# Optimization experiments

Hardware: AMD Instinct MI355X
Metric: run time of the kernel (lower is better)

## Reference

```python
import jax, jax.numpy as jnp
import numpy as np

N, C, H, W = 16, 512, 32, 32
NH = 8            # num_heads
HD = C // NH      # head dim c = 64
G = C // 4        # GroupNorm groups = 128
EPS = 1e-5


def conv1x1(X, Wt, b):
    # 1x1 Conv2d == per-pixel linear over channels
    return jnp.einsum('oc,nchw->nohw', Wt, X) + b[None, :, None, None]


def setup_inputs() -> dict:
    key = jax.random.key(0)
    ks = jax.random.split(key, 9)
    s = 0.02
    inp = {
        'X': jax.random.normal(ks[0], (N, C, H, W), jnp.float32),
        'Wq': jax.random.normal(ks[1], (C, C), jnp.float32) * s,
        'bq': jax.random.normal(ks[2], (C,), jnp.float32) * s,
        'Wk': jax.random.normal(ks[3], (C, C), jnp.float32) * s,
        'bk': jax.random.normal(ks[4], (C,), jnp.float32) * s,
        'Wv': jax.random.normal(ks[5], (C, C), jnp.float32) * s,
        'bv': jax.random.normal(ks[6], (C,), jnp.float32) * s,
        'Wo': jax.random.normal(ks[7], (C, C), jnp.float32) * s,
        'bo': jax.random.normal(ks[8], (C,), jnp.float32) * s,
        'gn_w': jnp.ones((C,), jnp.float32),
        'gn_b': jnp.zeros((C,), jnp.float32),
    }
    return inp


def reference(X, Wq, bq, Wk, bk, Wv, bv, Wo, bo, gn_w, gn_b):
    # NOTE: original torch code does  K, Q, V = (Q_conv(X), K_conv(X), V_conv(X))
    # i.e. K gets the Q_conv weights and Q gets the K_conv weights; mirror that.
    K = conv1x1(X, Wq, bq)
    Q = conv1x1(X, Wk, bk)
    V = conv1x1(X, Wv, bv)

    d = H * W
    Kh = K.reshape(N, NH, HD, d)  # [n,h,c,d]
    Qh = Q.reshape(N, NH, HD, d)
    Vh = V.reshape(N, NH, HD, d)

    # softmax-free channel attention: (Q^T K) then V (Q^T K)^T
    A = jnp.einsum('nhcd,nhcD->nhdD', Qh, Kh)   # [n,h,d,d]
    O = jnp.einsum('nhdD,nhcD->nhcd', A, Vh)    # [n,h,c,d]

    O = O.reshape(N, C, H, W)
    O = conv1x1(O, Wo, bo)

    # GroupNorm(G, C) with affine, eps=1e-5
    Og = O.reshape(N, G, C // G, H, W)
    mu = Og.mean(axis=(2, 3, 4), keepdims=True)
    var = Og.var(axis=(2, 3, 4), keepdims=True)
    On = ((Og - mu) * jax.lax.rsqrt(var + EPS)).reshape(N, C, H, W)
    On = On * gn_w[None, :, None, None] + gn_b[None, :, None, None]

    return On + X
```

## Files before the change

### kernel.cpp

```cpp
#include <hip/hip_runtime.h>
#include <hip/hip_bf16.h>

typedef __attribute__((ext_vector_type(8))) short s8v;
typedef __attribute__((ext_vector_type(4))) short s4v;
typedef __attribute__((ext_vector_type(4))) float f32x4;

#define MFMA_BF16 __builtin_amdgcn_mfma_f32_16x16x32_bf16

__device__ inline void gload_lds16(const __hip_bfloat16* g, __hip_bfloat16* l) {
  __builtin_amdgcn_global_load_lds(
      (const __attribute__((address_space(1))) void*)g,
      (__attribute__((address_space(3))) void*)l, 16, 0, 0);
}

__device__ inline short f2bs(float x) {
  __hip_bfloat16 b = __float2bfloat16(x);
  return *reinterpret_cast<short*>(&b);
}

__device__ inline void storeC(float* p, float v) { *p = v; }
__device__ inline void storeC(__hip_bfloat16* p, float v) { *p = __float2bfloat16(v); }

__global__ __launch_bounds__(256) void prep(const float* __restrict__ X,
                                            __hip_bfloat16* __restrict__ XT,
                                            const float* __restrict__ Wq,
                                            const float* __restrict__ Wv,
                                            const float* __restrict__ Wk,
                                            const float* __restrict__ Wo,
                                            const float* __restrict__ bq,
                                            const float* __restrict__ bv,
                                            __hip_bfloat16* __restrict__ WA,
                                            __hip_bfloat16* __restrict__ WkT,
                                            __hip_bfloat16* __restrict__ WOb,
                                            float* __restrict__ biasKV) {
  const int tid = threadIdx.x;
  if (blockIdx.z == 16) {
    const int blk = blockIdx.y * 16 + blockIdx.x;
#pragma unroll
    for (int t = 0; t < 8; ++t) {
      const int i = (blk * 8 + t) * 256 + tid;
      WA[i] = __float2bfloat16(Wq[i]);
      WA[262144 + i] = __float2bfloat16(Wv[i]);
      WOb[i] = __float2bfloat16(Wo[i]);
      WkT[i] = __float2bfloat16(Wk[(i & 511) * 512 + (i >> 9)]);
      if (i < 512) { biasKV[i] = bq[i]; biasKV[512 + i] = bv[i]; }
    }
    return;
  }
  __shared__ float tl[64][65];
  const int n = blockIdx.z;
  const int c0 = blockIdx.y * 64, p0 = blockIdx.x * 64;
  const int lr = tid >> 4, lc4 = (tid & 15) * 4;
  const float* Xp = X + ((long)n * 512 + c0) * 1024 + p0;
#pragma unroll
  for (int i = 0; i < 4; ++i) {
    const int ch = i * 16 + lr;
    const float4 v = *(const float4*)&Xp[(long)ch * 1024 + lc4];
    tl[ch][lc4 + 0] = v.x; tl[ch][lc4 + 1] = v.y;
    tl[ch][lc4 + 2] = v.z; tl[ch][lc4 + 3] = v.w;
  }
  __syncthreads();
  __hip_bfloat16* XTp = XT + ((long)n * 1024 + p0) * 512 + c0;
#pragma unroll
  for (int i = 0; i < 4; ++i) {
    const int px = i * 16 + lr;
    s4v o;
#pragma unroll
    for (int e = 0; e < 4; ++e) o[e] = f2bs(tl[lc4 + e][px]);
    *(s4v*)&XTp[(long)px * 512 + lc4] = o;
  }
}

template <typename OutT, bool BROW>
__global__ __launch_bounds__(256) void gemm_nt(
    const __hip_bfloat16* __restrict__ A, long strideA,
    const __hip_bfloat16* __restrict__ B, long strideB,
    OutT* __restrict__ C, long strideC, int K, int ldc,
    const float* __restrict__ brow, long strideBrow) {
  A += blockIdx.z * strideA;
  B += blockIdx.z * strideB;
  C += blockIdx.z * strideC;
  const int m0 = blockIdx.y * 128;
  const int n0 = blockIdx.x * 128;
  const int tid = threadIdx.x;
  const int wid = tid >> 6, lane = tid & 63;
  const int wm = wid >> 1, wn = wid & 1;

  __shared__ __hip_bfloat16 As[128 * 64];
  __shared__ __hip_bfloat16 Bs[128 * 64];

  f32x4 acc[4][4] = {};

  const __hip_bfloat16* gA0 = A + (long)(m0 + wid * 32 + (lane >> 3)) * K + (lane & 7) * 8;
  const __hip_bfloat16* gB0 = B + (long)(n0 + wid * 32 + (lane >> 3)) * K + (lane & 7) * 8;

  for (int k0 = 0; k0 < K; k0 += 64) {
#pragma unroll
    for (int t = 0; t < 4; ++t) {
      gload_lds16(gA0 + (long)t * 8 * K + k0, &As[(wid * 32 + t * 8) * 64]);
      gload_lds16(gB0 + (long)t * 8 * K + k0, &Bs[(wid * 32 + t * 8) * 64]);
    }
    __syncthreads();
#pragma unroll
    for (int ks = 0; ks < 2; ++ks) {
      const int koff = ks * 32 + (lane >> 4) * 8;
      s8v a[4], b[4];
#pragma unroll
      for (int i = 0; i < 4; ++i)
        a[i] = *(const s8v*)&As[(wm * 64 + i * 16 + (lane & 15)) * 64 + koff];
#pragma unroll
      for (int j = 0; j < 4; ++j)
        b[j] = *(const s8v*)&Bs[(wn * 64 + j * 16 + (lane & 15)) * 64 + koff];
#pragma unroll
      for (int i = 0; i < 4; ++i)
#pragma unroll
        for (int j = 0; j < 4; ++j)
          acc[i][j] = MFMA_BF16(a[i], b[j], acc[i][j], 0, 0, 0);
    }
    __syncthreads();
  }

  const int cr = (lane >> 4) * 4;
  const int cc = lane & 15;
#pragma unroll
  for (int i = 0; i < 4; ++i) {
#pragma unroll
    for (int r = 0; r < 4; ++r) {
      const int gm = m0 + wm * 64 + i * 16 + cr + r;
      const float rb = BROW ? brow[blockIdx.z * strideBrow + gm] : 0.f;
#pragma unroll
      for (int j = 0; j < 4; ++j) {
        const int gn = n0 + wn * 64 + j * 16 + cc;
        storeC(&C[(long)gm * ldc + gn], acc[i][j][r] + rb);
      }
    }
  }
}

__global__ __launch_bounds__(512) void gemm_vkT(const __hip_bfloat16* __restrict__ V,
                                                const __hip_bfloat16* __restrict__ Kk,
                                                __hip_bfloat16* __restrict__ Mt) {
  const int n = blockIdx.x >> 3, h = blockIdx.x & 7;
  const int tid = threadIdx.x, wid = tid >> 6, lane = tid & 63;
  f32x4 acc[4][4] = {};
  const long colbase = (long)n * 1024 + wid * 128 + (lane >> 4) * 8;
  const __hip_bfloat16* Vb = V + (long)(h * 64 + (lane & 15)) * 16384 + colbase;
  const __hip_bfloat16* Kb = Kk + (long)(h * 64 + (lane & 15)) * 16384 + colbase;
#pragma unroll
  for (int kk = 0; kk < 128; kk += 32) {
    s8v a[4], b[4];
#pragma unroll
    for (int i = 0; i < 4; ++i) a[i] = *(const s8v*)(Vb + (long)i * 16 * 16384 + kk);
#pragma unroll
    for (int j = 0; j < 4; ++j) b[j] = *(const s8v*)(Kb + (long)j * 16 * 16384 + kk);
#pragma unroll
    for (int i = 0; i < 4; ++i)
#pragma unroll
      for (int j = 0; j < 4; ++j) acc[i][j] = MFMA_BF16(a[i], b[j], acc[i][j], 0, 0, 0);
  }
  __shared__ float part[4][4096];
  const int cr = (lane >> 4) * 4, cc = lane & 15;
  if (wid < 4) {
#pragma unroll
    for (int i = 0; i < 4; ++i)
#pragma unroll
      for (int r = 0; r < 4; ++r)
#pragma unroll
        for (int j = 0; j < 4; ++j)
          part[wid][(i * 16 + cr + r) * 64 + j * 16 + cc] = acc[i][j][r];
  }
  __syncthreads();
  if (wid >= 4) {
#pragma unroll
    for (int i = 0; i < 4; ++i)
#pragma unroll
      for (int r = 0; r < 4; ++r)
#pragma unroll
        for (int j = 0; j < 4; ++j)
          part[wid - 4][(i * 16 + cr + r) * 64 + j * 16 + cc] += acc[i][j][r];
  }
  __syncthreads();
  __hip_bfloat16* outp = Mt + ((long)n * 8 + h) * 4096;
  for (int e = tid; e < 4096; e += 512) {
    const float sum = part[0][e] + part[1][e] + part[2][e] + part[3][e];
    outp[(e & 63) * 64 + (e >> 6)] = __float2bfloat16(sum);
  }
}

__global__ __launch_bounds__(256) void wchain(const __hip_bfloat16* __restrict__ WOb,
                                              const __hip_bfloat16* __restrict__ WkT,
                                              const __hip_bfloat16* __restrict__ Mt,
                                              const float* __restrict__ bk,
                                              const float* __restrict__ bo,
                                              __hip_bfloat16* __restrict__ WPP,
                                              float* __restrict__ b2out) {
  const int c0 = blockIdx.x * 128, o0 = blockIdx.y * 128, n = blockIdx.z;
  const int tid = threadIdx.x, wid = tid >> 6, lane = tid & 63;
  const int wm = wid >> 1, wn = wid & 1;
  const int cr = (lane >> 4) * 4, cc = lane & 15;

  __shared__ __hip_bfloat16 WoS[128 * 64];
  __shared__ __hip_bfloat16 WkS[128 * 64];
  __shared__ __hip_bfloat16 MtS[64 * 64];
  __shared__ __hip_bfloat16 W1S[128 * 64];
  __shared__ float bkS[512];

  if (tid < 128) *(float4*)&bkS[tid * 4] = *(const float4*)&bk[tid * 4];

  f32x4 acc2[4][4] = {};
  float bacc = 0.f;
  const int r8 = lane >> 3, b8 = (lane & 7) * 8;

  for (int h = 0; h < 8; ++h) {
#pragma unroll
    for (int t = 0; t < 4; ++t) {
      const int row = wid * 32 + t * 8;
      gload_lds16(WOb + (long)(o0 + row + r8) * 512 + h * 64 + b8, &WoS[row * 64]);
      gload_lds16(WkT + (long)(c0 + row + r8) * 512 + h * 64 + b8, &WkS[row * 64]);
    }
    {
      const __hip_bfloat16* mg = Mt + ((long)n * 8 + h) * 4096;
      gload_lds16(mg + wid * 512 + lane * 8, &MtS[wid * 512]);
      gload_lds16(mg + 2048 + wid * 512 + lane * 8, &MtS[2048 + wid * 512]);
    }
    __syncthreads();

    f32x4 acc1[2][4] = {};
#pragma unroll
    for (int ks = 0; ks < 2; ++ks) {
      const int ko = ks * 32 + (lane >> 4) * 8;
      s8v aj[2], bw[4];
#pragma unroll
      for (int i = 0; i < 2; ++i)
        aj[i] = *(const s8v*)&MtS[(wn * 32 + i * 16 + cc) * 64 + ko];
#pragma unroll
      for (int t = 0; t < 4; ++t)
        bw[t] = *(const s8v*)&WoS[(wm * 64 + t * 16 + cc) * 64 + ko];
#pragma unroll
      for (int i = 0; i < 2; ++i)
#pragma unroll
        for (int t = 0; t < 4; ++t)
          acc1[i][t] = MFMA_BF16(aj[i], bw[t], acc1[i][t], 0, 0, 0);
    }
#pragma unroll
    for (int i = 0; i < 2; ++i)
#pragma unroll
      for (int t = 0; t < 4; ++t) {
        const int o = wm * 64 + t * 16 + cc;
        const int jb = wn * 32 + i * 16 + cr;
        s4v p;
#pragma unroll
        for (int r = 0; r < 4; ++r) p[r] = f2bs(acc1[i][t][r]);
        *(s4v*)((char*)W1S + ((o * 128 + jb * 2) ^ ((o & 7) << 4))) = p;
      }
    __syncthreads();

#pragma unroll
    for (int ks = 0; ks < 2; ++ks) {
      const int ko = ks * 32 + (lane >> 4) * 8;
      s8v a2[4], bw[4];
#pragma unroll
      for (int i = 0; i < 4; ++i) {
        const int o = wm * 64 + i * 16 + cc;
        a2[i] = *(const s8v*)((char*)W1S + ((o * 128 + ko * 2) ^ ((o & 7) << 4)));
      }
#pragma unroll
      for (int t = 0; t < 4; ++t)
        bw[t] = *(const s8v*)&WkS[(wn * 64 + t * 16 + cc) * 64 + ko];
#pragma unroll
      for (int i = 0; i < 4; ++i)
#pragma unroll
        for (int t = 0; t < 4; ++t)
          acc2[i][t] = MFMA_BF16(a2[i], bw[t], acc2[i][t], 0, 0, 0);
    }

    if (c0 == 0) {
      const int o = tid >> 1, half = tid & 1;
      float s = 0.f;
#pragma unroll
      for (int q = 0; q < 4; ++q) {
        const int jb = half * 64 + q * 16;
        const s8v w = *(const s8v*)((char*)W1S + ((o * 128 + jb) ^ ((o & 7) << 4)));
        const __hip_bfloat16* wb = (const __hip_bfloat16*)&w;
#pragma unroll
        for (int e = 0; e < 8; ++e)
          s += __bfloat162float(wb[e]) * bkS[h * 64 + half * 32 + q * 8 + e];
      }
      bacc += s;
    }
    __syncthreads();
  }

#pragma unroll
  for (int i = 0; i < 4; ++i)
#pragma unroll
    for (int r = 0; r < 4; ++r)
#pragma unroll
      for (int t = 0; t < 4; ++t)
        WPP[((long)n * 512 + o0 + wm * 64 + i * 16 + cr + r) * 512 +
            c0 + wn * 64 + t * 16 + cc] = __float2bfloat16(acc2[i][t][r]);
  if (c0 == 0) {
    const float tot = bacc + __shfl_xor(bacc, 1);
    if ((tid & 1) == 0) {
      const int o = tid >> 1;
      b2out[n * 512 + o0 + o] = tot + bo[o0 + o];
    }
  }
}

__global__ __launch_bounds__(256) void gn_res(const __hip_bfloat16* __restrict__ Y,
                                              const float* __restrict__ X,
                                              const float* __restrict__ gw,
                                              const float* __restrict__ gb,
                                              float* __restrict__ out) {
  const int n = blockIdx.x >> 7, g = blockIdx.x & 127;
  const long base = ((long)n * 512 + g * 4) * 1024;
  const int tid = threadIdx.x;
  float v[16];
  float s = 0.f, s2 = 0.f;
#pragma unroll
  for (int i = 0; i < 2; ++i) {
    const s8v x = *(const s8v*)&Y[base + ((long)(i * 256 + tid)) * 8];
#pragma unroll
    for (int e = 0; e < 8; ++e) {
      const float f = __bfloat162float(((const __hip_bfloat16*)&x)[e]);
      v[i * 8 + e] = f;
      s += f;
      s2 += f * f;
    }
  }
#pragma unroll
  for (int off = 32; off; off >>= 1) {
    s += __shfl_down(s, off);
    s2 += __shfl_down(s2, off);
  }
  __shared__ float rs[8];
  const int wid = tid >> 6, lane = tid & 63;
  if (lane == 0) { rs[wid] = s; rs[4 + wid] = s2; }
  __syncthreads();
  if (tid == 0) {
    const float ts = rs[0] + rs[1] + rs[2] + rs[3];
    const float t2 = rs[4] + rs[5] + rs[6] + rs[7];
    const float mu = ts * (1.f / 4096.f);
    const float var = t2 * (1.f / 4096.f) - mu * mu;
    rs[0] = mu;
    rs[1] = rsqrtf(var + 1e-5f);
  }
  __syncthreads();
  const float mu = rs[0], rstd = rs[1];
#pragma unroll
  for (int i = 0; i < 2; ++i) {
    const int chunk = i * 256 + tid;
    const long e0 = base + (long)chunk * 8;
    const int c = g * 4 + (chunk >> 7);
    const float sc = rstd * gw[c], sh = gb[c];
    const float4 x0 = *(const float4*)&X[e0];
    const float4 x1 = *(const float4*)&X[e0 + 4];
    float4 o0, o1;
    o0.x = (v[i * 8 + 0] - mu) * sc + sh + x0.x;
    o0.y = (v[i * 8 + 1] - mu) * sc + sh + x0.y;
    o0.z = (v[i * 8 + 2] - mu) * sc + sh + x0.z;
    o0.w = (v[i * 8 + 3] - mu) * sc + sh + x0.w;
    o1.x = (v[i * 8 + 4] - mu) * sc + sh + x1.x;
    o1.y = (v[i * 8 + 5] - mu) * sc + sh + x1.y;
    o1.z = (v[i * 8 + 6] - mu) * sc + sh + x1.z;
    o1.w = (v[i * 8 + 7] - mu) * sc + sh + x1.w;
    *(float4*)&out[e0] = o0;
    *(float4*)&out[e0 + 4] = o1;
  }
}

extern "C" void kernel_launch(void* const* d_in, const int* in_sizes, int n_in,
                              void* d_out, int out_size, void* d_ws, size_t ws_size,
                              hipStream_t stream) {
  const float* X  = (const float*)d_in[0];
  const float* Wq = (const float*)d_in[1];
  const float* bq = (const float*)d_in[2];
  const float* Wk = (const float*)d_in[3];
  const float* bk = (const float*)d_in[4];
  const float* Wv = (const float*)d_in[5];
  const float* bv = (const float*)d_in[6];
  const float* Wo = (const float*)d_in[7];
  const float* bo = (const float*)d_in[8];
  const float* gw = (const float*)d_in[9];
  const float* gb = (const float*)d_in[10];
  float* out = (float*)d_out;

  char* ws = (char*)d_ws;
  __hip_bfloat16* XT  = (__hip_bfloat16*)(ws + 0);
  __hip_bfloat16* KV  = (__hip_bfloat16*)(ws + 16777216);
  __hip_bfloat16* Y   = (__hip_bfloat16*)(ws + 16777216);
  __hip_bfloat16* WPP = (__hip_bfloat16*)(ws + 58720256);
  __hip_bfloat16* Mt  = (__hip_bfloat16*)(ws + 67108864);
  __hip_bfloat16* WA  = (__hip_bfloat16*)(ws + 68157440);
  __hip_bfloat16* WkT = (__hip_bfloat16*)(ws + 69206016);
  __hip_bfloat16* WOb = (__hip_bfloat16*)(ws + 69730304);
  float*          bKV = (float*)(ws + 70254592);
  float*          b2  = (float*)(ws + 70258688);

  prep<<<dim3(16, 8, 17), 256, 0, stream>>>(X, XT, Wq, Wv, Wk, Wo, bq, bv,
                                            WA, WkT, WOb, bKV);
  gemm_nt<__hip_bfloat16, true><<<dim3(128, 8, 1), 256, 0, stream>>>(
      WA, 0, XT, 0, KV, 0, 512, 16384, bKV, 0);
  gemm_vkT<<<128, 512, 0, stream>>>(KV + (long)512 * 16384, KV, Mt);
  wchain<<<dim3(4, 4, 16), 256, 0, stream>>>(WOb, WkT, Mt, bk, bo, WPP, b2);
  gemm_nt<__hip_bfloat16, true><<<dim3(8, 4, 16), 256, 0, stream>>>(
      WPP, 262144, XT, 524288, Y, 524288, 512, 1024, b2, 512);
  gn_res<<<2048, 256, 0, stream>>>(Y, X, gw, gb, out);
}
```

Measured before the change: 117.2 us.

## Split VK^T reduction across two blocks, XCD-swizzle QKV GEMM, narrow final GEMM tiles

gemm_vkT now launches twice as many blocks. Each one reduces half of the spatial dimension and writes fp32 partials, and wchain sums the two halves and converts them to bf16 when loading into LDS. The first GEMM gets a 1D grid with an XCD-aware block remap so that blocks sharing data land on the same chiplet's L2. The final batched GEMM uses 128x64 tiles, giving twice as many blocks and better CU occupancy. The costs are extra fp32 partial traffic and a smaller MFMA work-per-load ratio in the narrowed GEMM.

```diff
diff --git a/kernel.cpp b/kernel.cpp
--- a/kernel.cpp
+++ b/kernel.cpp
@@ -71,50 +71,61 @@
   }
 }
 
-template <typename OutT, bool BROW>
+template <typename OutT, bool BROW, int NJ, int SWZ>
 __global__ __launch_bounds__(256) void gemm_nt(
     const __hip_bfloat16* __restrict__ A, long strideA,
     const __hip_bfloat16* __restrict__ B, long strideB,
     OutT* __restrict__ C, long strideC, int K, int ldc,
     const float* __restrict__ brow, long strideBrow) {
-  A += blockIdx.z * strideA;
-  B += blockIdx.z * strideB;
-  C += blockIdx.z * strideC;
-  const int m0 = blockIdx.y * 128;
-  const int n0 = blockIdx.x * 128;
+  int bx, by, bz;
+  if (SWZ == 1) {
+    const int id = blockIdx.x;
+    const int xcd = id & 7, local = id >> 3;
+    bx = xcd * 16 + (local >> 3);
+    by = local & 7;
+    bz = 0;
+  } else {
+    bx = blockIdx.x; by = blockIdx.y; bz = blockIdx.z;
+  }
+  A += bz * strideA;
+  B += bz * strideB;
+  C += bz * strideC;
+  const int m0 = by * 128;
+  const int n0 = bx * (32 * NJ);
   const int tid = threadIdx.x;
   const int wid = tid >> 6, lane = tid & 63;
   const int wm = wid >> 1, wn = wid & 1;
 
   __shared__ __hip_bfloat16 As[128 * 64];
-  __shared__ __hip_bfloat16 Bs[128 * 64];
-
-  f32x4 acc[4][4] = {};
+  __shared__ __hip_bfloat16 Bs[32 * NJ * 64];
+
+  f32x4 acc[4][NJ] = {};
 
   const __hip_bfloat16* gA0 = A + (long)(m0 + wid * 32 + (lane >> 3)) * K + (lane & 7) * 8;
-  const __hip_bfloat16* gB0 = B + (long)(n0 + wid * 32 + (lane >> 3)) * K + (lane & 7) * 8;
+  const __hip_bfloat16* gB0 = B + (long)(n0 + wid * 8 * NJ + (lane >> 3)) * K + (lane & 7) * 8;
 
   for (int k0 = 0; k0 < K; k0 += 64) {
 #pragma unroll
-    for (int t = 0; t < 4; ++t) {
+    for (int t = 0; t < 4; ++t)
       gload_lds16(gA0 + (long)t * 8 * K + k0, &As[(wid * 32 + t * 8) * 64]);
-      gload_lds16(gB0 + (long)t * 8 * K + k0, &Bs[(wid * 32 + t * 8) * 64]);
-    }
+#pragma unroll
+    for (int t = 0; t < NJ; ++t)
+      gload_lds16(gB0 + (long)t * 8 * K + k0, &Bs[(wid * 8 * NJ + t * 8) * 64]);
     __syncthreads();
 #pragma unroll
     for (int ks = 0; ks < 2; ++ks) {
       const int koff = ks * 32 + (lane >> 4) * 8;
-      s8v a[4], b[4];
+      s8v a[4], b[NJ];
 #pragma unroll
       for (int i = 0; i < 4; ++i)
         a[i] = *(const s8v*)&As[(wm * 64 + i * 16 + (lane & 15)) * 64 + koff];
 #pragma unroll
-      for (int j = 0; j < 4; ++j)
-        b[j] = *(const s8v*)&Bs[(wn * 64 + j * 16 + (lane & 15)) * 64 + koff];
+      for (int j = 0; j < NJ; ++j)
+        b[j] = *(const s8v*)&Bs[(wn * 16 * NJ + j * 16 + (lane & 15)) * 64 + koff];
 #pragma unroll
       for (int i = 0; i < 4; ++i)
 #pragma unroll
-        for (int j = 0; j < 4; ++j)
+        for (int j = 0; j < NJ; ++j)
           acc[i][j] = MFMA_BF16(a[i], b[j], acc[i][j], 0, 0, 0);
     }
     __syncthreads();
@@ -127,10 +138,10 @@
 #pragma unroll
     for (int r = 0; r < 4; ++r) {
       const int gm = m0 + wm * 64 + i * 16 + cr + r;
-      const float rb = BROW ? brow[blockIdx.z * strideBrow + gm] : 0.f;
-#pragma unroll
-      for (int j = 0; j < 4; ++j) {
-        const int gn = n0 + wn * 64 + j * 16 + cc;
+      const float rb = BROW ? brow[bz * strideBrow + gm] : 0.f;
+#pragma unroll
+      for (int j = 0; j < NJ; ++j) {
+        const int gn = n0 + wn * 16 * NJ + j * 16 + cc;
         storeC(&C[(long)gm * ldc + gn], acc[i][j][r] + rb);
       }
     }
@@ -139,15 +150,16 @@
 
 __global__ __launch_bounds__(512) void gemm_vkT(const __hip_bfloat16* __restrict__ V,
                                                 const __hip_bfloat16* __restrict__ Kk,
-                                                __hip_bfloat16* __restrict__ Mt) {
-  const int n = blockIdx.x >> 3, h = blockIdx.x & 7;
+                                                float* __restrict__ Part) {
+  const int bx = blockIdx.x;
+  const int n = bx >> 4, h = (bx >> 1) & 7, half = bx & 1;
   const int tid = threadIdx.x, wid = tid >> 6, lane = tid & 63;
   f32x4 acc[4][4] = {};
-  const long colbase = (long)n * 1024 + wid * 128 + (lane >> 4) * 8;
+  const long colbase = (long)n * 1024 + half * 512 + wid * 64 + (lane >> 4) * 8;
   const __hip_bfloat16* Vb = V + (long)(h * 64 + (lane & 15)) * 16384 + colbase;
   const __hip_bfloat16* Kb = Kk + (long)(h * 64 + (lane & 15)) * 16384 + colbase;
 #pragma unroll
-  for (int kk = 0; kk < 128; kk += 32) {
+  for (int kk = 0; kk < 64; kk += 32) {
     s8v a[4], b[4];
 #pragma unroll
     for (int i = 0; i < 4; ++i) a[i] = *(const s8v*)(Vb + (long)i * 16 * 16384 + kk);
@@ -180,16 +192,16 @@
           part[wid - 4][(i * 16 + cr + r) * 64 + j * 16 + cc] += acc[i][j][r];
   }
   __syncthreads();
-  __hip_bfloat16* outp = Mt + ((long)n * 8 + h) * 4096;
+  float* outp = Part + (long)bx * 4096;
   for (int e = tid; e < 4096; e += 512) {
     const float sum = part[0][e] + part[1][e] + part[2][e] + part[3][e];
-    outp[(e & 63) * 64 + (e >> 6)] = __float2bfloat16(sum);
+    outp[(e & 63) * 64 + (e >> 6)] = sum;
   }
 }
 
 __global__ __launch_bounds__(256) void wchain(const __hip_bfloat16* __restrict__ WOb,
                                               const __hip_bfloat16* __restrict__ WkT,
-                                              const __hip_bfloat16* __restrict__ Mt,
+                                              const float* __restrict__ Part,
                                               const float* __restrict__ bk,
                                               const float* __restrict__ bo,
                                               __hip_bfloat16* __restrict__ WPP,
@@ -219,9 +231,17 @@
       gload_lds16(WkT + (long)(c0 + row + r8) * 512 + h * 64 + b8, &WkS[row * 64]);
     }
     {
-      const __hip_bfloat16* mg = Mt + ((long)n * 8 + h) * 4096;
-      gload_lds16(mg + wid * 512 + lane * 8, &MtS[wid * 512]);
-      gload_lds16(mg + 2048 + wid * 512 + lane * 8, &MtS[2048 + wid * 512]);
+      const float* P0 = Part + (long)((n * 8 + h) * 2) * 4096;
+#pragma unroll
+      for (int q = 0; q < 4; ++q) {
+        const int e = tid * 16 + q * 4;
+        const float4 a = *(const float4*)&P0[e];
+        const float4 b = *(const float4*)&P0[4096 + e];
+        s4v o;
+        o[0] = f2bs(a.x + b.x); o[1] = f2bs(a.y + b.y);
+        o[2] = f2bs(a.z + b.z); o[3] = f2bs(a.w + b.w);
+        *(s4v*)&MtS[e] = o;
+      }
     }
     __syncthreads();
 
@@ -387,24 +407,24 @@
   float* out = (float*)d_out;
 
   char* ws = (char*)d_ws;
-  __hip_bfloat16* XT  = (__hip_bfloat16*)(ws + 0);
-  __hip_bfloat16* KV  = (__hip_bfloat16*)(ws + 16777216);
-  __hip_bfloat16* Y   = (__hip_bfloat16*)(ws + 16777216);
-  __hip_bfloat16* WPP = (__hip_bfloat16*)(ws + 58720256);
-  __hip_bfloat16* Mt  = (__hip_bfloat16*)(ws + 67108864);
-  __hip_bfloat16* WA  = (__hip_bfloat16*)(ws + 68157440);
-  __hip_bfloat16* WkT = (__hip_bfloat16*)(ws + 69206016);
-  __hip_bfloat16* WOb = (__hip_bfloat16*)(ws + 69730304);
-  float*          bKV = (float*)(ws + 70254592);
-  float*          b2  = (float*)(ws + 70258688);
+  __hip_bfloat16* XT   = (__hip_bfloat16*)(ws + 0);
+  __hip_bfloat16* KV   = (__hip_bfloat16*)(ws + 16777216);
+  __hip_bfloat16* Y    = (__hip_bfloat16*)(ws + 16777216);
+  __hip_bfloat16* WPP  = (__hip_bfloat16*)(ws + 58720256);
+  float*          Part = (float*)(ws + 67108864);
+  __hip_bfloat16* WA   = (__hip_bfloat16*)(ws + 71303168);
+  __hip_bfloat16* WkT  = (__hip_bfloat16*)(ws + 72351744);
+  __hip_bfloat16* WOb  = (__hip_bfloat16*)(ws + 72876032);
+  float*          bKV  = (float*)(ws + 73400320);
+  float*          b2   = (float*)(ws + 73404416);
 
   prep<<<dim3(16, 8, 17), 256, 0, stream>>>(X, XT, Wq, Wv, Wk, Wo, bq, bv,
                                             WA, WkT, WOb, bKV);
-  gemm_nt<__hip_bfloat16, true><<<dim3(128, 8, 1), 256, 0, stream>>>(
+  gemm_nt<__hip_bfloat16, true, 4, 1><<<1024, 256, 0, stream>>>(
       WA, 0, XT, 0, KV, 0, 512, 16384, bKV, 0);
-  gemm_vkT<<<128, 512, 0, stream>>>(KV + (long)512 * 16384, KV, Mt);
-  wchain<<<dim3(4, 4, 16), 256, 0, stream>>>(WOb, WkT, Mt, bk, bo, WPP, b2);
-  gemm_nt<__hip_bfloat16, true><<<dim3(8, 4, 16), 256, 0, stream>>>(
+  gemm_vkT<<<256, 512, 0, stream>>>(KV + (long)512 * 16384, KV, Part);
+  wchain<<<dim3(4, 4, 16), 256, 0, stream>>>(WOb, WkT, Part, bk, bo, WPP, b2);
+  gemm_nt<__hip_bfloat16, true, 2, 0><<<dim3(16, 4, 16), 256, 0, stream>>>(
       WPP, 262144, XT, 524288, Y, 524288, 512, 1024, b2, 512);
   gn_res<<<2048, 256, 0, stream>>>(Y, X, gw, gb, out);
 }
```

Result: slower. 120.9 us (+3.1%).
